# Kernel optimization log

Measured on AMD Instinct MI355X. Metric: run time of the kernel, lower is better.

## Reference

```python
import jax, jax.numpy as jnp
import numpy as np

EPS = 1e-6

def _conv1x1(x, w, bias):
    # x: [b,cin,h,w], w: [cout,cin]
    y = jnp.einsum('bchw,oc->bohw', x, w)
    return y + bias[None, :, None, None]

def _maxpool2(x):
    b, c, h, w = x.shape
    return x.reshape(b, c, h // 2, 2, w // 2, 2).max(axis=(3, 5))

def _up2_align_corners(x):
    # bilinear upsample x2, align_corners=True (matches torch nn.Upsample)
    b, c, h, w = x.shape
    oh, ow = 2 * h, 2 * w
    ys = jnp.linspace(0.0, h - 1.0, oh)
    xs = jnp.linspace(0.0, w - 1.0, ow)
    y0 = jnp.floor(ys).astype(jnp.int32); y1 = jnp.minimum(y0 + 1, h - 1)
    x0 = jnp.floor(xs).astype(jnp.int32); x1 = jnp.minimum(x0 + 1, w - 1)
    ty = (ys - y0).reshape(1, 1, oh, 1)
    tx = (xs - x0).reshape(1, 1, 1, ow)
    r0 = x[:, :, y0, :]; r1 = x[:, :, y1, :]           # [b,c,oh,w]
    v00 = r0[:, :, :, x0]; v01 = r0[:, :, :, x1]       # [b,c,oh,ow]
    v10 = r1[:, :, :, x0]; v11 = r1[:, :, :, x1]
    return (1 - ty) * ((1 - tx) * v00 + tx * v01) + ty * ((1 - tx) * v10 + tx * v11)

def _norm_corr(fm):
    # fm: [b,N,N], indexed [b,p,q]; ReLU then L2-normalize over q for each p
    m = jnp.maximum(fm, 0.0)
    norm = jnp.sqrt(jnp.sum(m * m, axis=2, keepdims=True) + EPS)
    return m / norm

def setup_inputs() -> dict:
    key = jax.random.key(0)
    ks = jax.random.split(key, 8)
    d = {
        'xa': jax.random.normal(ks[0], (8, 256, 64, 64), jnp.float32),
        'xb': jax.random.normal(ks[1], (8, 256, 64, 64), jnp.float32),
        'conv_w': jax.random.normal(ks[2], (1024, 256), jnp.float32) * 0.02,
        'conv_b': jax.random.normal(ks[3], (1024,), jnp.float32) * 0.02,
        'We': jax.random.normal(ks[4], (1024, 1024), jnp.float32) * 0.02,
        'We2': jax.random.normal(ks[5], (1024, 1024), jnp.float32) * 0.02,
        'conv2_w': jax.random.normal(ks[6], (256, 1024), jnp.float32) * 0.02,
        'conv2_b': jax.random.normal(ks[7], (256,), jnp.float32) * 0.02,
    }
    return d

def reference(xa, xb, conv_w, conv_b, We, We2, conv2_w, conv2_b):
    fa = _maxpool2(_conv1x1(xa, conv_w, conv_b))   # [b,c,h,w]
    fb = _maxpool2(_conv1x1(xb, conv_w, conv_b))
    b, c, h, w = fa.shape
    N = h * w
    Fa = fa.reshape(b, c, N)                        # [b,c,N]
    Fb = fb.reshape(b, c, N)
    Fb_t = jnp.swapaxes(Fb, 1, 2)                   # [b,N,c]
    Fa_t = jnp.swapaxes(Fa, 1, 2)
    # fm[b,p,q] = (linear_e(Fb_t) @ Fa)
    fm = jnp.einsum('bpc,cd,bdq->bpq', Fb_t, We.T, Fa)
    Mab = _norm_corr(fm)                            # normalized over q per p
    fm2 = jnp.einsum('bpc,cd,bdq->bpq', Fa_t, We2.T, Fb)
    Mba = _norm_corr(fm2)
    # torch: bmm(corr.view(b,N,N), feat) with corr_flat[b,q,p] = Mn[b,p,q]
    en_a = jnp.einsum('bpq,bpk->bqk', Mab, Fa_t)    # [b,N,c]
    en_b = jnp.einsum('bpq,bpk->bqk', Mba, Fb_t)
    # faithful reinterpretation (torch .view(b,c,h,w) on a [b,N,c] tensor)
    en_a = en_a.reshape(b, c, h, w)
    en_b = en_b.reshape(b, c, h, w)
    en_a = _conv1x1(_up2_align_corners(en_a), conv2_w, conv2_b)
    en_b = _conv1x1(_up2_align_corners(en_b), conv2_w, conv2_b)
    return (en_a, en_b)
```

## Files before the change

### kernel.cpp

```cpp
#include <hip/hip_runtime.h>

typedef unsigned short u16;
typedef short bfrag __attribute__((ext_vector_type(8)));
typedef float facc  __attribute__((ext_vector_type(4)));

__device__ __forceinline__ float bf2f(u16 u) {
    union { unsigned int i; float f; } v; v.i = ((unsigned int)u) << 16; return v.f;
}
__device__ __forceinline__ u16 f2bf(float f) {
    union { float f; unsigned int i; } v; v.f = f;
    unsigned int r = v.i + 0x7FFFu + ((v.i >> 16) & 1u);
    return (u16)(r >> 16);
}

__device__ __forceinline__ void store_out(u16* p, float v)   { *p = f2bf(v); }
__device__ __forceinline__ void store_out(float* p, float v) { *p = v; }

__device__ __forceinline__ void gl2lds16(const u16* g, char* l) {
    __builtin_amdgcn_global_load_lds(
        (const __attribute__((address_space(1))) unsigned int*)g,
        (__attribute__((address_space(3))) unsigned int*)l,
        16, 0, 0);
}

__global__ void cvt4_k(const float* __restrict__ s0, u16* __restrict__ d0,
                       const float* __restrict__ s1, u16* __restrict__ d1,
                       const float* __restrict__ s2, u16* __restrict__ d2,
                       const float* __restrict__ s3, u16* __restrict__ d3) {
    int i = blockIdx.x * blockDim.x + threadIdx.x;
    if (i < 262144)        d0[i] = f2bf(s0[i]);
    else if (i < 1310720)  d1[i - 262144] = f2bf(s1[i - 262144]);
    else if (i < 2359296)  d2[i - 1310720] = f2bf(s2[i - 1310720]);
    else                   d3[i - 2359296] = f2bf(s3[i - 2359296]);
}

__global__ void transpose_in_k(const float* __restrict__ srcA,
                               const float* __restrict__ srcB,
                               u16* __restrict__ dst) {
    __shared__ u16 tile[64][65];
    const long SX = 1048576;
    const int z  = blockIdx.z;
    const int c0 = blockIdx.x * 64;
    const int r0 = blockIdx.y * 64;
    const int x  = threadIdx.x;
    const int y0 = threadIdx.y;
    const float* s = (z < 8 ? srcA : srcB) + (size_t)(z & 7) * SX;
    for (int i = 0; i < 8; ++i) {
        int r = y0 + i * 8;
        tile[r][x] = f2bf(s[(size_t)(r0 + r) * 4096 + c0 + x]);
    }
    __syncthreads();
    u16* d = dst + (size_t)z * SX;
    for (int i = 0; i < 8; ++i) {
        int c = y0 + i * 8;
        d[(size_t)(c0 + c) * 256 + r0 + x] = tile[x][c];
    }
}

template <typename OutT, int MODE, bool PAIRED>
__global__ __launch_bounds__(256)
void gemm_nt(const u16* __restrict__ A0, const u16* __restrict__ A1, long strideA,
             const u16* __restrict__ B0, const u16* __restrict__ B1, long strideBT,
             OutT* __restrict__ C, long strideC, u16* __restrict__ CT,
             const float* __restrict__ bias, int M, int N, int K) {
    __shared__ __align__(16) char smem[32768];
    char* As = smem;
    char* Bs = smem + 16384;

    const int gx = gridDim.x, gy = gridDim.y;
    long id = blockIdx.x + (long)gx * (blockIdx.y + (long)gy * blockIdx.z);
    long total = (long)gx * gy * gridDim.z;
    long nid = (id & 7) * (total >> 3) + (id >> 3);
    const int bx = (int)(nid % gx);
    long rr = nid / gx;
    const int by = (int)(rr % gy);
    const int b  = (int)(rr / gy);

    const int m0 = bx * 128;
    const int n0 = by * 128;

    const u16* Ab; const u16* Bb;
    if (PAIRED) {
        const int bl = b & 7;
        Ab = (b < 8 ? A0 : A1) + (size_t)bl * strideA;
        Bb = (b < 8 ? B0 : B1) + (size_t)bl * strideBT;
    } else {
        Ab = A0 + (size_t)b * strideA;
        Bb = B0 + (size_t)b * strideBT;
    }

    const int t    = threadIdx.x;
    const int lane = t & 63;
    const int w    = t >> 6;
    const int wm   = (w & 1) * 64;
    const int wn   = (w >> 1) * 64;
    const int q    = lane >> 4;
    const int ln   = lane & 15;

    const int s0 = w * 64 + lane;
    const int s1 = s0 + 256;
    const int r0s = s0 >> 2, c0s = (s0 & 3) * 8;
    const int r1s = s1 >> 2, c1s = (s1 & 3) * 8;

    const u16* pA0 = Ab + (size_t)(m0 + r0s) * K + c0s;
    const u16* pA1 = Ab + (size_t)(m0 + r1s) * K + c1s;
    const u16* pB0 = Bb + (size_t)(n0 + r0s) * K + c0s;
    const u16* pB1 = Bb + (size_t)(n0 + r1s) * K + c1s;

    facc acc[4][4];
    for (int i = 0; i < 4; ++i)
        for (int j = 0; j < 4; ++j)
            acc[i][j] = (facc)0.0f;

    const int nK = K >> 6;
    for (int kt = 0; kt < nK; ++kt) {
        const int k0 = kt << 6;
        gl2lds16(pA0 + k0,      As + s0 * 16);
        gl2lds16(pA1 + k0,      As + s1 * 16);
        gl2lds16(pA0 + k0 + 32, As + 8192 + s0 * 16);
        gl2lds16(pA1 + k0 + 32, As + 8192 + s1 * 16);
        gl2lds16(pB0 + k0,      Bs + s0 * 16);
        gl2lds16(pB1 + k0,      Bs + s1 * 16);
        gl2lds16(pB0 + k0 + 32, Bs + 8192 + s0 * 16);
        gl2lds16(pB1 + k0 + 32, Bs + 8192 + s1 * 16);
        __syncthreads();
        for (int j = 0; j < 2; ++j) {
            const char* Aj = As + j * 8192;
            const char* Bj = Bs + j * 8192;
            bfrag af[4], bfr[4];
            for (int mt = 0; mt < 4; ++mt)
                af[mt] = *reinterpret_cast<const bfrag*>(Aj + (wm + mt * 16 + ln) * 64 + q * 16);
            for (int nt = 0; nt < 4; ++nt)
                bfr[nt] = *reinterpret_cast<const bfrag*>(Bj + (wn + nt * 16 + ln) * 64 + q * 16);
            for (int mt = 0; mt < 4; ++mt)
                for (int nt = 0; nt < 4; ++nt)
                    acc[mt][nt] = __builtin_amdgcn_mfma_f32_16x16x32_bf16(af[mt], bfr[nt], acc[mt][nt], 0, 0, 0);
        }
        __syncthreads();
    }

    if (MODE == 0) {
        u16* Cb = (u16*)C + (size_t)b * strideC;
        u16* dump = (u16*)smem;
        for (int mt = 0; mt < 4; ++mt)
            for (int nt = 0; nt < 4; ++nt)
                for (int r = 0; r < 4; ++r)
                    dump[(wm + mt * 16 + q * 4 + r) * 128 + wn + nt * 16 + ln] = f2bf(acc[mt][nt][r]);
        __syncthreads();
        for (int i = 0; i < 8; ++i) {
            const int row = w * 32 + i * 4 + (lane >> 4);
            const uint4 v = *reinterpret_cast<const uint4*>(dump + row * 128 + (lane & 15) * 8);
            *reinterpret_cast<uint4*>(Cb + (size_t)(m0 + row) * N + n0 + (lane & 15) * 8) = v;
        }
    } else {
        OutT* Cb = C + (size_t)b * strideC;
        for (int mt = 0; mt < 4; ++mt) {
            const int rbase = m0 + wm + mt * 16 + q * 4;
            for (int nt = 0; nt < 4; ++nt) {
                const int col = n0 + wn + nt * 16 + ln;
                for (int r = 0; r < 4; ++r)
                    store_out(&Cb[(size_t)(rbase + r) * N + col], acc[mt][nt][r] + bias[rbase + r]);
            }
        }
    }
}

#define BARP() do { asm volatile("" ::: "memory"); __builtin_amdgcn_s_barrier(); asm volatile("" ::: "memory"); } while (0)
#define VM4P() asm volatile("s_waitcnt vmcnt(4)" ::: "memory")
#define VM0P() asm volatile("s_waitcnt vmcnt(0)" ::: "memory")

#define STGP(KT, BUF) do { \
    gl2lds16(pA0 + (KT) * 32, smem + (BUF) * 16384 + s0 * 16); \
    gl2lds16(pA1 + (KT) * 32, smem + (BUF) * 16384 + s1 * 16); \
    gl2lds16(pB0 + (KT) * 32, smem + (BUF) * 16384 + 8192 + s0 * 16); \
    gl2lds16(pB1 + (KT) * 32, smem + (BUF) * 16384 + 8192 + s1 * 16); \
} while (0)

__global__ __launch_bounds__(256)
void gemm2p_pool(const u16* __restrict__ A, const u16* __restrict__ B0, long strideBT,
                 u16* __restrict__ C, long strideC, u16* __restrict__ CT,
                 const float* __restrict__ bias, int K) {
    __shared__ __align__(16) char smem[32768];

    const int gx = gridDim.x, gy = gridDim.y;
    long id = blockIdx.x + (long)gx * (blockIdx.y + (long)gy * blockIdx.z);
    long total = (long)gx * gy * gridDim.z;
    long nid = (id & 7) * (total >> 3) + (id >> 3);
    const int bx = (int)(nid % gx);
    long rr = nid / gx;
    const int by = (int)(rr % gy);
    const int b  = (int)(rr / gy);
    const int m0 = bx * 128;

    const u16* Bb = B0 + (size_t)b * strideBT;

    const int t    = threadIdx.x;
    const int lane = t & 63;
    const int w    = t >> 6;
    const int wm   = (w & 1) * 64;
    const int wn   = (w >> 1) * 64;
    const int q    = lane >> 4;
    const int ln   = lane & 15;

    const int s0 = w * 64 + lane;
    const int s1 = s0 + 256;
    const int r0s = s0 >> 2, c0s = s0 & 3;
    const int r1s = s1 >> 2, c1s = s1 & 3;
    const int x0 = (r0s >> 1) & 3, x1 = (r1s >> 1) & 3;
    const int gr0 = (2 * by + ((r0s >> 1) & 1)) * 64 + (r0s >> 2) * 2 + (r0s & 1);
    const int gr1 = (2 * by + ((r1s >> 1) & 1)) * 64 + (r1s >> 2) * 2 + (r1s & 1);

    const u16* pA0 = A  + (size_t)(m0 + r0s) * K + (c0s ^ x0) * 8;
    const u16* pA1 = A  + (size_t)(m0 + r1s) * K + (c1s ^ x1) * 8;
    const u16* pB0 = Bb + (size_t)gr0 * K + (c0s ^ x0) * 8;
    const u16* pB1 = Bb + (size_t)gr1 * K + (c1s ^ x1) * 8;

    facc acc[4][4];
    #pragma unroll
    for (int i = 0; i < 4; ++i)
        #pragma unroll
        for (int j = 0; j < 4; ++j)
            acc[i][j] = (facc)0.0f;

    const int nK = K >> 5;

    STGP(0, 0);
    for (int kt = 0; kt < nK; ++kt) {
        const bool more = (kt + 1 < nK);
        if (more) { STGP(kt + 1, (kt + 1) & 1); VM4P(); } else { VM0P(); }
        BARP();
        const char* Aj = smem + (kt & 1) * 16384;
        const char* Bj = Aj + 8192;
        bfrag af[4], bfr[4];
        #pragma unroll
        for (int mt = 0; mt < 4; ++mt) {
            const int row = wm + mt * 16 + ln;
            af[mt] = *reinterpret_cast<const bfrag*>(Aj + row * 64 + ((q ^ ((row >> 1) & 3)) << 4));
        }
        #pragma unroll
        for (int nt = 0; nt < 4; ++nt) {
            const int row = wn + nt * 16 + ln;
            bfr[nt] = *reinterpret_cast<const bfrag*>(Bj + row * 64 + ((q ^ ((row >> 1) & 3)) << 4));
        }
        #pragma unroll
        for (int mt = 0; mt < 4; ++mt)
            #pragma unroll
            for (int nt = 0; nt < 4; ++nt)
                acc[mt][nt] = __builtin_amdgcn_mfma_f32_16x16x32_bf16(af[mt], bfr[nt], acc[mt][nt], 0, 0, 0);
        BARP();
    }

    u16* Cp  = C  + (size_t)b * strideC;
    u16* CTb = CT + (size_t)b * strideC;
    const int a = ln >> 2;
    #pragma unroll
    for (int mt = 0; mt < 4; ++mt) {
        const int chb = wm + mt * 16 + q * 4;
        float bs0 = bias[m0 + chb + 0];
        float bs1 = bias[m0 + chb + 1];
        float bs2 = bias[m0 + chb + 2];
        float bs3 = bias[m0 + chb + 3];
        #pragma unroll
        for (int nt = 0; nt < 4; ++nt) {
            const int xp = (wn >> 2) + nt * 4 + a;
            float p0 = acc[mt][nt][0] + bs0;
            float p1 = acc[mt][nt][1] + bs1;
            float p2 = acc[mt][nt][2] + bs2;
            float p3 = acc[mt][nt][3] + bs3;
            p0 = fmaxf(p0, __shfl_xor(p0, 1, 64)); p0 = fmaxf(p0, __shfl_xor(p0, 2, 64));
            p1 = fmaxf(p1, __shfl_xor(p1, 1, 64)); p1 = fmaxf(p1, __shfl_xor(p1, 2, 64));
            p2 = fmaxf(p2, __shfl_xor(p2, 1, 64)); p2 = fmaxf(p2, __shfl_xor(p2, 2, 64));
            p3 = fmaxf(p3, __shfl_xor(p3, 1, 64)); p3 = fmaxf(p3, __shfl_xor(p3, 2, 64));
            float s01 = (ln & 1) ? p1 : p0;
            float s23 = (ln & 1) ? p3 : p2;
            float sel = (ln & 2) ? s23 : s01;
            Cp[(size_t)(m0 + chb + (ln & 3)) * 1024 + by * 32 + xp] = f2bf(sel);
            if ((ln & 3) == 0) {
                uint2 pk;
                pk.x = (unsigned)f2bf(p0) | ((unsigned)f2bf(p1) << 16);
                pk.y = (unsigned)f2bf(p2) | ((unsigned)f2bf(p3) << 16);
                *reinterpret_cast<uint2*>(&CTb[(size_t)(by * 32 + xp) * 1024 + m0 + chb]) = pk;
            }
        }
    }
}

#define BAR8() do { asm volatile("" ::: "memory"); __builtin_amdgcn_s_barrier(); asm volatile("" ::: "memory"); } while (0)
#define VM6() asm volatile("s_waitcnt vmcnt(6)" ::: "memory")
#define VM0() asm volatile("s_waitcnt vmcnt(0)" ::: "memory")

#define LDA8(BUF, MH) \
    _Pragma("unroll") for (int mf = 0; mf < 4; ++mf) { \
        _Pragma("unroll") for (int ks = 0; ks < 2; ++ks) \
            a[mf][ks] = *reinterpret_cast<const bfrag*>(Ab8 + (BUF) * 32768 + \
                (wr * 128 + ((MH) * 4 + mf) * 16 + ln) * 128 + (((ks * 4 + q) ^ ln7) << 4)); }

#define LDB8(BUF, NH) \
    _Pragma("unroll") for (int nf = 0; nf < 2; ++nf) { \
        _Pragma("unroll") for (int ks = 0; ks < 2; ++ks) \
            bb[(NH) * 2 + nf][ks] = *reinterpret_cast<const bfrag*>(Bb8 + (BUF) * 32768 + \
                (wc * 64 + ((NH) * 2 + nf) * 16 + ln) * 128 + (((ks * 4 + q) ^ ln7) << 4)); }

#define MM8(MH, NH) \
    _Pragma("unroll") for (int mf = 0; mf < 4; ++mf) \
    _Pragma("unroll") for (int nf = 0; nf < 2; ++nf) \
    _Pragma("unroll") for (int ks = 0; ks < 2; ++ks) \
        acc[(MH) * 4 + mf][(NH) * 2 + nf] = __builtin_amdgcn_mfma_f32_16x16x32_bf16( \
            a[mf][ks], bb[(NH) * 2 + nf][ks], acc[(MH) * 4 + mf][(NH) * 2 + nf], 0, 0, 0);

#define STA8(KT, BUF, H, R) gl2lds16(pAs + (size_t)((H) * 128 + (R) * 8) * K + (KT) * 64, \
        Ab8 + (BUF) * 32768 + (H) * 16384 + (w * 2 + (R)) * 1024 + lane * 16)
#define STB8(KT, BUF, H, R) gl2lds16(pBs + (size_t)((H) * 128 + (R) * 8) * K + (KT) * 64, \
        Bb8 + (BUF) * 32768 + (H) * 16384 + (w * 2 + (R)) * 1024 + lane * 16)

template <bool PAIRED>
__global__ __launch_bounds__(512, 1)
void gemm8_nt(const u16* __restrict__ A0, const u16* __restrict__ A1, long strideA,
              const u16* __restrict__ B0, const u16* __restrict__ B1, long strideBT,
              u16* __restrict__ C, long strideC, int N, int K) {
    __shared__ __align__(16) char smem8[131072];
    char* Ab8 = smem8;
    char* Bb8 = smem8 + 65536;

    const int gx = gridDim.x, gy = gridDim.y;
    long id = blockIdx.x + (long)gx * (blockIdx.y + (long)gy * blockIdx.z);
    long total = (long)gx * gy * gridDim.z;
    long nid = (id & 7) * (total >> 3) + (id >> 3);
    const int bx = (int)(nid % gx);
    long rr = nid / gx;
    const int by = (int)(rr % gy);
    const int b  = (int)(rr / gy);
    const int m0 = bx * 256, n0 = by * 256;

    const u16* Ab; const u16* Bb;
    if (PAIRED) {
        const int bl = b & 7;
        Ab = (b < 8 ? A0 : A1) + (size_t)bl * strideA;
        Bb = (b < 8 ? B0 : B1) + (size_t)bl * strideBT;
    } else {
        Ab = A0 + (size_t)b * strideA;
        Bb = B0 + (size_t)b * strideBT;
    }

    const int t    = threadIdx.x;
    const int lane = t & 63;
    const int w    = t >> 6;
    const int wr   = w >> 2;
    const int wc   = w & 3;
    const int q    = lane >> 4;
    const int ln   = lane & 15;
    const int ln7  = ln & 7;
    const int l8   = lane >> 3;
    const int l7   = lane & 7;

    const u16* pAs = Ab + (size_t)(m0 + w * 16 + l8) * K + (l7 ^ l8) * 8;
    const u16* pBs = Bb + (size_t)(n0 + w * 16 + l8) * K + (l7 ^ l8) * 8;

    facc acc[8][4];
    #pragma unroll
    for (int i = 0; i < 8; ++i)
        #pragma unroll
        for (int j = 0; j < 4; ++j)
            acc[i][j] = (facc)0.0f;

    bfrag a[4][2];
    bfrag bb[4][2];

    const int nIter = K >> 7;

    STB8(0, 0, 0, 0); STB8(0, 0, 0, 1); STB8(0, 0, 1, 0); STB8(0, 0, 1, 1);
    STA8(0, 0, 0, 0); STA8(0, 0, 0, 1); STA8(0, 0, 1, 0); STA8(0, 0, 1, 1);
    STB8(1, 1, 0, 0); STB8(1, 1, 0, 1); STB8(1, 1, 1, 0); STB8(1, 1, 1, 1);
    STA8(1, 1, 0, 0); STA8(1, 1, 0, 1);
    VM6();
    BAR8();

    for (int i = 0; i < nIter; ++i) {
        const bool more = (i + 1 < nIter);
        const int t1 = 2 * i + 1, t2 = 2 * i + 2, t3 = 2 * i + 3;

        LDA8(0, 0); LDB8(0, 0);
        STA8(t1, 1, 1, 0); STA8(t1, 1, 1, 1);
        BAR8();
        __builtin_amdgcn_s_setprio(1); MM8(0, 0); __builtin_amdgcn_s_setprio(0);
        BAR8();
        LDB8(0, 1);
        BAR8();
        __builtin_amdgcn_s_setprio(1); MM8(0, 1); __builtin_amdgcn_s_setprio(0);
        BAR8();
        LDA8(0, 1);
        if (more) { STB8(t2, 0, 0, 0); STB8(t2, 0, 0, 1); STB8(t2, 0, 1, 0); STB8(t2, 0, 1, 1); }
        BAR8();
        __builtin_amdgcn_s_setprio(1); MM8(1, 0); __builtin_amdgcn_s_setprio(0);
        BAR8();
        if (more) { STA8(t2, 0, 0, 0); STA8(t2, 0, 0, 1); VM6(); } else { VM0(); }
        BAR8();
        __builtin_amdgcn_s_setprio(1); MM8(1, 1); __builtin_amdgcn_s_setprio(0);
        BAR8();
        LDA8(1, 0); LDB8(1, 0);
        if (more) { STA8(t2, 0, 1, 0); STA8(t2, 0, 1, 1); }
        BAR8();
        __builtin_amdgcn_s_setprio(1); MM8(0, 0); __builtin_amdgcn_s_setprio(0);
        BAR8();
        LDB8(1, 1);
        BAR8();
        __builtin_amdgcn_s_setprio(1); MM8(0, 1); __builtin_amdgcn_s_setprio(0);
        BAR8();
        LDA8(1, 1);
        if (more) { STB8(t3, 1, 0, 0); STB8(t3, 1, 0, 1); STB8(t3, 1, 1, 0); STB8(t3, 1, 1, 1); }
        BAR8();
        __builtin_amdgcn_s_setprio(1); MM8(1, 0); __builtin_amdgcn_s_setprio(0);
        BAR8();
        if (more) { STA8(t3, 1, 0, 0); STA8(t3, 1, 0, 1); VM6(); } else { VM0(); }
        BAR8();
        __builtin_amdgcn_s_setprio(1); MM8(1, 1); __builtin_amdgcn_s_setprio(0);
        BAR8();
    }

    u16* dump = (u16*)smem8;
    #pragma unroll
    for (int mf = 0; mf < 8; ++mf)
        #pragma unroll
        for (int nf = 0; nf < 4; ++nf)
            #pragma unroll
            for (int r = 0; r < 4; ++r)
                dump[(wr * 128 + mf * 16 + q * 4 + r) * 256 + wc * 64 + nf * 16 + ln] =
                    f2bf(acc[mf][nf][r]);
    BAR8();
    u16* Cb = C + (size_t)b * strideC;
    #pragma unroll
    for (int it = 0; it < 16; ++it) {
        int linear = t + it * 512;
        int row = linear >> 5, c16 = linear & 31;
        uint4 v = *reinterpret_cast<const uint4*>(dump + row * 256 + c16 * 8);
        *reinterpret_cast<uint4*>(Cb + (size_t)(m0 + row) * N + n0 + c16 * 8) = v;
    }
}

__global__ void norm_rk(const u16* __restrict__ fm, float* __restrict__ rinv) {
    __shared__ float red[4];
    const long row = blockIdx.x;
    const u16* p = fm + row * 1024;
    const int t = threadIdx.x;
    uint2 raw = *reinterpret_cast<const uint2*>(p + t * 4);
    float v0 = fmaxf(bf2f((u16)(raw.x & 0xFFFF)), 0.f);
    float v1 = fmaxf(bf2f((u16)(raw.x >> 16)), 0.f);
    float v2 = fmaxf(bf2f((u16)(raw.y & 0xFFFF)), 0.f);
    float v3 = fmaxf(bf2f((u16)(raw.y >> 16)), 0.f);
    float s = v0 * v0 + v1 * v1 + v2 * v2 + v3 * v3;
    for (int off = 32; off; off >>= 1) s += __shfl_down(s, off, 64);
    if ((t & 63) == 0) red[t >> 6] = s;
    __syncthreads();
    if (t == 0)
        rinv[row] = 1.0f / sqrtf(red[0] + red[1] + red[2] + red[3] + 1e-6f);
}

__global__ void transpose_scale_k(const u16* __restrict__ src,
                                  const float* __restrict__ rinv,
                                  u16* __restrict__ dst) {
    __shared__ u16 tile[64][65];
    const long S = 1048576;
    const int b  = blockIdx.z;
    const int c0 = blockIdx.x * 64;
    const int r0 = blockIdx.y * 64;
    const int x  = threadIdx.x;
    const int y0 = threadIdx.y;
    const u16* s = src + (size_t)b * S;
    const float* rv = rinv + (size_t)b * 1024;
    for (int i = 0; i < 8; ++i) {
        int r = y0 + i * 8;
        float v = fmaxf(bf2f(s[(size_t)(r0 + r) * 1024 + c0 + x]), 0.f) * rv[r0 + r];
        tile[r][x] = f2bf(v);
    }
    __syncthreads();
    u16* d = dst + (size_t)b * S;
    for (int i = 0; i < 8; ++i) {
        int c = y0 + i * 8;
        d[(size_t)(c0 + c) * 1024 + r0 + x] = tile[x][c];
    }
}

__global__ void upsample_k(const float* __restrict__ V, float* __restrict__ out, int total) {
    int idx = blockIdx.x * blockDim.x + threadIdx.x;
    if (idx >= total) return;
    int X  = idx & 63;
    int Y  = (idx >> 6) & 63;
    long bo = idx >> 12;
    const float* p = V + bo * 1024;
    const float sc = 31.0f / 63.0f;
    float ys = Y * sc;
    float xs = X * sc;
    int y0 = (int)ys; int x0 = (int)xs;
    int y1 = y0 + 1; if (y1 > 31) y1 = 31;
    int x1 = x0 + 1; if (x1 > 31) x1 = 31;
    float ty = ys - y0, tx = xs - x0;
    float v00 = p[y0 * 32 + x0], v01 = p[y0 * 32 + x1];
    float v10 = p[y1 * 32 + x0], v11 = p[y1 * 32 + x1];
    out[idx] = (1.f - ty) * ((1.f - tx) * v00 + tx * v01) + ty * ((1.f - tx) * v10 + tx * v11);
}

extern "C" void kernel_launch(void* const* d_in, const int* in_sizes, int n_in,
                              void* d_out, int out_size, void* d_ws, size_t ws_size,
                              hipStream_t stream) {
    const float* xa      = (const float*)d_in[0];
    const float* xb      = (const float*)d_in[1];
    const float* conv_w  = (const float*)d_in[2];
    const float* conv_b  = (const float*)d_in[3];
    const float* We      = (const float*)d_in[4];
    const float* We2     = (const float*)d_in[5];
    const float* conv2_w = (const float*)d_in[6];
    const float* conv2_b = (const float*)d_in[7];
    float* out = (float*)d_out;
    char* ws = (char*)d_ws;

    const long S1M = 1048576;
    const long MiB = 1048576;

    u16*   XT  = (u16*)(ws + 0);
    u16*   T1  = (u16*)(ws + 0);
    u16*   MT  = (u16*)(ws + 0);
    u16*   FA  = (u16*)(ws + 32 * MiB);
    u16*   FB  = (u16*)(ws + 48 * MiB);
    u16*   FAT = (u16*)(ws + 64 * MiB);
    u16*   FBT = (u16*)(ws + 80 * MiB);
    float* V   = (float*)(ws + 64 * MiB);
    u16*   FM  = (u16*)(ws + 96 * MiB);
    u16*   Z   = (u16*)(ws + 96 * MiB);
    u16*   CW  = (u16*)(ws + 128 * MiB);
    u16*   WE  = (u16*)(ws + 128 * MiB + 524288);
    u16*   WE2 = (u16*)(ws + 128 * MiB + 2621440);
    u16*   C2W = (u16*)(ws + 128 * MiB + 4718592);
    float* RIV = (float*)(ws + 128 * MiB + 5242880);

    const dim3 tb64(64, 8);

    cvt4_k<<<10240, 256, 0, stream>>>(conv_w, CW, We, WE, We2, WE2, conv2_w, C2W);

    transpose_in_k<<<dim3(64, 4, 16), tb64, 0, stream>>>(xa, xb, XT);

    gemm2p_pool<<<dim3(8, 32, 16), 256, 0, stream>>>(
        CW, XT, S1M, FA, S1M, FAT, conv_b, 256);

    gemm8_nt<true><<<dim3(4, 4, 16), 512, 0, stream>>>(
        FBT, FAT, S1M, WE, WE2, 0, T1, S1M, 1024, 1024);

    gemm8_nt<true><<<dim3(4, 4, 16), 512, 0, stream>>>(
        T1, T1 + 8 * S1M, S1M, FAT, FBT, S1M, FM, S1M, 1024, 1024);

    norm_rk<<<16384, 256, 0, stream>>>(FM, RIV);

    transpose_scale_k<<<dim3(16, 16, 16), tb64, 0, stream>>>(FM, RIV, MT);

    gemm8_nt<true><<<dim3(4, 4, 16), 512, 0, stream>>>(
        FA, FB, S1M, MT, MT + 8 * S1M, S1M, Z, S1M, 1024, 1024);

    gemm_nt<float, 1, false><<<dim3(2, 8, 16), 256, 0, stream>>>(
        C2W, C2W, 0, Z, Z, S1M, V, 256L * 1024, nullptr, conv2_b, 256, 1024, 1024);

    upsample_k<<<65536, 256, 0, stream>>>(V, out, 16 * 256 * 4096);
}
```

Before: 369.8 us.

## Replace 256x256 eight-wave GEMM with 128x128 triple-buffered four-wave kernel

The three batched 1024x1024x1024 GEMMs switch from a 512-thread kernel with 256x256 tiles and a hand-interleaved ping-pong schedule to a 256-thread kernel with 128x128 tiles. The new kernel uses a 3-stage LDS ring with K-step 32 and a simple wait/barrier per step. This gives 1024 blocks instead of 256, improving CU occupancy and wave balance on the device. The cost is lower data reuse per tile, more global/L2 traffic, and less tuned overlap than the previous schedule.

```diff
diff --git a/kernel.cpp b/kernel.cpp
--- a/kernel.cpp
+++ b/kernel.cpp
@@ -166,6 +166,7 @@
 }
 
 #define BARP() do { asm volatile("" ::: "memory"); __builtin_amdgcn_s_barrier(); asm volatile("" ::: "memory"); } while (0)
+#define VM8P() asm volatile("s_waitcnt vmcnt(8)" ::: "memory")
 #define VM4P() asm volatile("s_waitcnt vmcnt(4)" ::: "memory")
 #define VM0P() asm volatile("s_waitcnt vmcnt(0)" ::: "memory")
 
@@ -285,42 +286,12 @@
     }
 }
 
-#define BAR8() do { asm volatile("" ::: "memory"); __builtin_amdgcn_s_barrier(); asm volatile("" ::: "memory"); } while (0)
-#define VM6() asm volatile("s_waitcnt vmcnt(6)" ::: "memory")
-#define VM0() asm volatile("s_waitcnt vmcnt(0)" ::: "memory")
-
-#define LDA8(BUF, MH) \
-    _Pragma("unroll") for (int mf = 0; mf < 4; ++mf) { \
-        _Pragma("unroll") for (int ks = 0; ks < 2; ++ks) \
-            a[mf][ks] = *reinterpret_cast<const bfrag*>(Ab8 + (BUF) * 32768 + \
-                (wr * 128 + ((MH) * 4 + mf) * 16 + ln) * 128 + (((ks * 4 + q) ^ ln7) << 4)); }
-
-#define LDB8(BUF, NH) \
-    _Pragma("unroll") for (int nf = 0; nf < 2; ++nf) { \
-        _Pragma("unroll") for (int ks = 0; ks < 2; ++ks) \
-            bb[(NH) * 2 + nf][ks] = *reinterpret_cast<const bfrag*>(Bb8 + (BUF) * 32768 + \
-                (wc * 64 + ((NH) * 2 + nf) * 16 + ln) * 128 + (((ks * 4 + q) ^ ln7) << 4)); }
-
-#define MM8(MH, NH) \
-    _Pragma("unroll") for (int mf = 0; mf < 4; ++mf) \
-    _Pragma("unroll") for (int nf = 0; nf < 2; ++nf) \
-    _Pragma("unroll") for (int ks = 0; ks < 2; ++ks) \
-        acc[(MH) * 4 + mf][(NH) * 2 + nf] = __builtin_amdgcn_mfma_f32_16x16x32_bf16( \
-            a[mf][ks], bb[(NH) * 2 + nf][ks], acc[(MH) * 4 + mf][(NH) * 2 + nf], 0, 0, 0);
-
-#define STA8(KT, BUF, H, R) gl2lds16(pAs + (size_t)((H) * 128 + (R) * 8) * K + (KT) * 64, \
-        Ab8 + (BUF) * 32768 + (H) * 16384 + (w * 2 + (R)) * 1024 + lane * 16)
-#define STB8(KT, BUF, H, R) gl2lds16(pBs + (size_t)((H) * 128 + (R) * 8) * K + (KT) * 64, \
-        Bb8 + (BUF) * 32768 + (H) * 16384 + (w * 2 + (R)) * 1024 + lane * 16)
-
 template <bool PAIRED>
-__global__ __launch_bounds__(512, 1)
-void gemm8_nt(const u16* __restrict__ A0, const u16* __restrict__ A1, long strideA,
-              const u16* __restrict__ B0, const u16* __restrict__ B1, long strideBT,
-              u16* __restrict__ C, long strideC, int N, int K) {
-    __shared__ __align__(16) char smem8[131072];
-    char* Ab8 = smem8;
-    char* Bb8 = smem8 + 65536;
+__global__ __launch_bounds__(256)
+void gemm3b_nt(const u16* __restrict__ A0, const u16* __restrict__ A1, long strideA,
+               const u16* __restrict__ B0, const u16* __restrict__ B1, long strideBT,
+               u16* __restrict__ C, long strideC, int N, int K) {
+    __shared__ __align__(16) char smem[49152];
 
     const int gx = gridDim.x, gy = gridDim.y;
     long id = blockIdx.x + (long)gx * (blockIdx.y + (long)gy * blockIdx.z);
@@ -330,7 +301,7 @@
     long rr = nid / gx;
     const int by = (int)(rr % gy);
     const int b  = (int)(rr / gy);
-    const int m0 = bx * 256, n0 = by * 256;
+    const int m0 = bx * 128, n0 = by * 128;
 
     const u16* Ab; const u16* Bb;
     if (PAIRED) {
@@ -345,95 +316,83 @@
     const int t    = threadIdx.x;
     const int lane = t & 63;
     const int w    = t >> 6;
-    const int wr   = w >> 2;
-    const int wc   = w & 3;
+    const int wm   = (w & 1) * 64;
+    const int wn   = (w >> 1) * 64;
     const int q    = lane >> 4;
     const int ln   = lane & 15;
-    const int ln7  = ln & 7;
-    const int l8   = lane >> 3;
-    const int l7   = lane & 7;
-
-    const u16* pAs = Ab + (size_t)(m0 + w * 16 + l8) * K + (l7 ^ l8) * 8;
-    const u16* pBs = Bb + (size_t)(n0 + w * 16 + l8) * K + (l7 ^ l8) * 8;
-
-    facc acc[8][4];
+
+    const int s0 = w * 64 + lane;
+    const int s1 = s0 + 256;
+    const int r0s = s0 >> 2, c0s = s0 & 3;
+    const int r1s = s1 >> 2, c1s = s1 & 3;
+    const int x0 = (r0s >> 1) & 3, x1 = (r1s >> 1) & 3;
+
+    const u16* pA0 = Ab + (size_t)(m0 + r0s) * K + (c0s ^ x0) * 8;
+    const u16* pA1 = Ab + (size_t)(m0 + r1s) * K + (c1s ^ x1) * 8;
+    const u16* pB0 = Bb + (size_t)(n0 + r0s) * K + (c0s ^ x0) * 8;
+    const u16* pB1 = Bb + (size_t)(n0 + r1s) * K + (c1s ^ x1) * 8;
+
+    facc acc[4][4];
     #pragma unroll
-    for (int i = 0; i < 8; ++i)
+    for (int i = 0; i < 4; ++i)
         #pragma unroll
         for (int j = 0; j < 4; ++j)
             acc[i][j] = (facc)0.0f;
 
-    bfrag a[4][2];
-    bfrag bb[4][2];
-
-    const int nIter = K >> 7;
-
-    STB8(0, 0, 0, 0); STB8(0, 0, 0, 1); STB8(0, 0, 1, 0); STB8(0, 0, 1, 1);
-    STA8(0, 0, 0, 0); STA8(0, 0, 0, 1); STA8(0, 0, 1, 0); STA8(0, 0, 1, 1);
-    STB8(1, 1, 0, 0); STB8(1, 1, 0, 1); STB8(1, 1, 1, 0); STB8(1, 1, 1, 1);
-    STA8(1, 1, 0, 0); STA8(1, 1, 0, 1);
-    VM6();
-    BAR8();
-
-    for (int i = 0; i < nIter; ++i) {
-        const bool more = (i + 1 < nIter);
-        const int t1 = 2 * i + 1, t2 = 2 * i + 2, t3 = 2 * i + 3;
-
-        LDA8(0, 0); LDB8(0, 0);
-        STA8(t1, 1, 1, 0); STA8(t1, 1, 1, 1);
-        BAR8();
-        __builtin_amdgcn_s_setprio(1); MM8(0, 0); __builtin_amdgcn_s_setprio(0);
-        BAR8();
-        LDB8(0, 1);
-        BAR8();
-        __builtin_amdgcn_s_setprio(1); MM8(0, 1); __builtin_amdgcn_s_setprio(0);
-        BAR8();
-        LDA8(0, 1);
-        if (more) { STB8(t2, 0, 0, 0); STB8(t2, 0, 0, 1); STB8(t2, 0, 1, 0); STB8(t2, 0, 1, 1); }
-        BAR8();
-        __builtin_amdgcn_s_setprio(1); MM8(1, 0); __builtin_amdgcn_s_setprio(0);
-        BAR8();
-        if (more) { STA8(t2, 0, 0, 0); STA8(t2, 0, 0, 1); VM6(); } else { VM0(); }
-        BAR8();
-        __builtin_amdgcn_s_setprio(1); MM8(1, 1); __builtin_amdgcn_s_setprio(0);
-        BAR8();
-        LDA8(1, 0); LDB8(1, 0);
-        if (more) { STA8(t2, 0, 1, 0); STA8(t2, 0, 1, 1); }
-        BAR8();
-        __builtin_amdgcn_s_setprio(1); MM8(0, 0); __builtin_amdgcn_s_setprio(0);
-        BAR8();
-        LDB8(1, 1);
-        BAR8();
-        __builtin_amdgcn_s_setprio(1); MM8(0, 1); __builtin_amdgcn_s_setprio(0);
-        BAR8();
-        LDA8(1, 1);
-        if (more) { STB8(t3, 1, 0, 0); STB8(t3, 1, 0, 1); STB8(t3, 1, 1, 0); STB8(t3, 1, 1, 1); }
-        BAR8();
-        __builtin_amdgcn_s_setprio(1); MM8(1, 0); __builtin_amdgcn_s_setprio(0);
-        BAR8();
-        if (more) { STA8(t3, 1, 0, 0); STA8(t3, 1, 0, 1); VM6(); } else { VM0(); }
-        BAR8();
-        __builtin_amdgcn_s_setprio(1); MM8(1, 1); __builtin_amdgcn_s_setprio(0);
-        BAR8();
-    }
-
-    u16* dump = (u16*)smem8;
+    const int nK = K >> 5;
+
+    STGP(0, 0);
+    STGP(1, 1);
+    int cb = 0;
+    for (int kt = 0; kt < nK; ++kt) {
+        const int rem = nK - 1 - kt;
+        if (rem >= 2) {
+            int sb = cb + 2; if (sb >= 3) sb -= 3;
+            STGP(kt + 2, sb);
+            VM8P();
+        } else if (rem == 1) {
+            VM4P();
+        } else {
+            VM0P();
+        }
+        BARP();
+        const char* Aj = smem + cb * 16384;
+        const char* Bj = Aj + 8192;
+        bfrag af[4], bfr[4];
+        #pragma unroll
+        for (int mt = 0; mt < 4; ++mt) {
+            const int row = wm + mt * 16 + ln;
+            af[mt] = *reinterpret_cast<const bfrag*>(Aj + row * 64 + ((q ^ ((row >> 1) & 3)) << 4));
+        }
+        #pragma unroll
+        for (int nt = 0; nt < 4; ++nt) {
+            const int row = wn + nt * 16 + ln;
+            bfr[nt] = *reinterpret_cast<const bfrag*>(Bj + row * 64 + ((q ^ ((row >> 1) & 3)) << 4));
+        }
+        #pragma unroll
+        for (int mt = 0; mt < 4; ++mt)
+            #pragma unroll
+            for (int nt = 0; nt < 4; ++nt)
+                acc[mt][nt] = __builtin_amdgcn_mfma_f32_16x16x32_bf16(af[mt], bfr[nt], acc[mt][nt], 0, 0, 0);
+        BARP();
+        ++cb; if (cb == 3) cb = 0;
+    }
+
+    u16* Cb = C + (size_t)b * strideC;
+    u16* dump = (u16*)smem;
     #pragma unroll
-    for (int mf = 0; mf < 8; ++mf)
-        #pragma unroll
-        for (int nf = 0; nf < 4; ++nf)
+    for (int mt = 0; mt < 4; ++mt)
+        #pragma unroll
+        for (int nt = 0; nt < 4; ++nt)
             #pragma unroll
             for (int r = 0; r < 4; ++r)
-                dump[(wr * 128 + mf * 16 + q * 4 + r) * 256 + wc * 64 + nf * 16 + ln] =
-                    f2bf(acc[mf][nf][r]);
-    BAR8();
-    u16* Cb = C + (size_t)b * strideC;
+                dump[(wm + mt * 16 + q * 4 + r) * 128 + wn + nt * 16 + ln] = f2bf(acc[mt][nt][r]);
+    __syncthreads();
     #pragma unroll
-    for (int it = 0; it < 16; ++it) {
-        int linear = t + it * 512;
-        int row = linear >> 5, c16 = linear & 31;
-        uint4 v = *reinterpret_cast<const uint4*>(dump + row * 256 + c16 * 8);
-        *reinterpret_cast<uint4*>(Cb + (size_t)(m0 + row) * N + n0 + c16 * 8) = v;
+    for (int i = 0; i < 8; ++i) {
+        const int row = w * 32 + i * 4 + (lane >> 4);
+        const uint4 v = *reinterpret_cast<const uint4*>(dump + row * 128 + (lane & 15) * 8);
+        *reinterpret_cast<uint4*>(Cb + (size_t)(m0 + row) * N + n0 + (lane & 15) * 8) = v;
     }
 }
 
@@ -541,17 +500,17 @@
     gemm2p_pool<<<dim3(8, 32, 16), 256, 0, stream>>>(
         CW, XT, S1M, FA, S1M, FAT, conv_b, 256);
 
-    gemm8_nt<true><<<dim3(4, 4, 16), 512, 0, stream>>>(
+    gemm3b_nt<true><<<dim3(8, 8, 16), 256, 0, stream>>>(
         FBT, FAT, S1M, WE, WE2, 0, T1, S1M, 1024, 1024);
 
-    gemm8_nt<true><<<dim3(4, 4, 16), 512, 0, stream>>>(
+    gemm3b_nt<true><<<dim3(8, 8, 16), 256, 0, stream>>>(
         T1, T1 + 8 * S1M, S1M, FAT, FBT, S1M, FM, S1M, 1024, 1024);
 
     norm_rk<<<16384, 256, 0, stream>>>(FM, RIV);
 
     transpose_scale_k<<<dim3(16, 16, 16), tb64, 0, stream>>>(FM, RIV, MT);
 
-    gemm8_nt<true><<<dim3(4, 4, 16), 512, 0, stream>>>(
+    gemm3b_nt<true><<<dim3(8, 8, 16), 256, 0, stream>>>(
         FA, FB, S1M, MT, MT + 8 * S1M, S1M, Z, S1M, 1024, 1024);
 
     gemm_nt<float, 1, false><<<dim3(2, 8, 16), 256, 0, stream>>>(
```

Result: slower. 410.6 us (+11.1%).
